# Kernel optimization log

Measured on AMD Instinct MI355X. Metric: run time of the kernel, lower is better.

## Reference

```python
import jax, jax.numpy as jnp
import numpy as np

BETA = 0.5

def setup_inputs() -> dict:
    key = jax.random.key(0)
    ks = jax.random.split(key, 10)
    B, H = 4096, 200
    ITEM, REGION = 100000, 1000
    D, HID = 128, 64  # embed_size, hidden_size
    half = D // 2
    history = jax.random.randint(ks[0], (B, H), 0, ITEM)
    target = jax.random.randint(ks[1], (B,), 0, ITEM)
    history_region = jax.random.randint(ks[2], (B, H), 0, REGION)
    target_region = jax.random.randint(ks[3], (B,), 0, REGION)
    W_hist = jax.random.normal(ks[4], (ITEM, half), jnp.float32) * 0.01
    W_tgt = jax.random.normal(ks[5], (ITEM, half), jnp.float32) * 0.01
    W_reg = jax.random.normal(ks[6], (REGION, half), jnp.float32) * 0.01
    W1 = jax.random.normal(ks[7], (D, HID), jnp.float32) * (1.0 / np.sqrt(D))
    b1 = jnp.zeros((HID,), jnp.float32)
    W2 = jax.random.normal(ks[8], (HID,), jnp.float32) * (1.0 / np.sqrt(HID))
    return {"history": history, "target": target,
            "history_region": history_region, "target_region": target_region,
            "W_hist": W_hist, "W_tgt": W_tgt, "W_reg": W_reg,
            "W1": W1, "b1": b1, "W2": W2}

def reference(history, target, history_region, target_region,
              W_hist, W_tgt, W_reg, W1, b1, W2):
    # gather + concat: [B,H,D] and [B,D]
    h = jnp.concatenate([W_hist[history], W_reg[history_region]], axis=-1)
    t = jnp.concatenate([W_tgt[target], W_reg[target_region]], axis=-1)
    inp = h * t[:, None, :]                      # [B,H,D]
    r1 = jax.nn.relu(inp @ W1 + b1)              # [B,H,HID] (dropout = identity at eval)
    logits = r1 @ W2                             # [B,H]
    mask = (history != target[:, None]).astype(logits.dtype)
    exp_A = jnp.exp(logits) * mask               # [B,H]
    exp_sum = jnp.sum(exp_A, axis=-1) ** BETA    # [B], beta-power normalization
    attn = exp_A / exp_sum[:, None]              # [B,H]
    pred = jnp.einsum('bhd,bd->b', h * attn[..., None], t)
    return jax.nn.sigmoid(pred)
```

## Files before the change

kernel.cpp:

```cpp
#include <hip/hip_runtime.h>
#include <math.h>

#define NB        4096
#define NH        200
#define HIST_ROWS 100000
#define REG_ROWS  1000
#define NTILES    13

typedef __attribute__((ext_vector_type(4))) int int4i;

#define SA 2048.0f
#define SB 16384.0f
#define ST 2048.0f
#define INV_LOGIT (1.0f / (SA * SB))
#define INV_S     (1.0f / (SA * ST))

__device__ __forceinline__ int q8(float x, float s) {
    return __float2int_rn(fminf(fmaxf(x * s, -127.f), 127.f));
}
__device__ __forceinline__ int pack4(float a, float b, float c, float d, float s) {
    const int x0 = q8(a, s), x1 = q8(b, s), x2 = q8(c, s), x3 = q8(d, s);
    return (x0 & 255) | ((x1 & 255) << 8) | ((x2 & 255) << 16) | (x3 << 24);
}

__global__ __launch_bounds__(256) void prep_all(
    const int*   __restrict__ target,
    const int*   __restrict__ target_region,
    const float* __restrict__ Wh, const float* __restrict__ Wr,
    const float* __restrict__ Wt, const float* __restrict__ W1,
    unsigned char* __restrict__ tab, signed char* __restrict__ Ball)
{
    if (blockIdx.x < NB) {
        const int b    = blockIdx.x;
        const int tgt  = target[b];
        const int treg = target_region[b];
        #pragma unroll
        for (int v = 0; v < 3; ++v) {
            const int i = threadIdx.x + v * 256;
            if (i < 640) {
                const int frag = i >> 6, nt = frag >> 1, ks = frag & 1;
                const int c = i & 63, q = c >> 4, l = c & 15;
                const float* tp = ks ? (Wr + (size_t)treg * 64) : (Wt + (size_t)tgt * 64);
                const float4 t0 = *(const float4*)(tp + q * 16);
                const float4 t1 = *(const float4*)(tp + q * 16 + 4);
                const float4 t2 = *(const float4*)(tp + q * 16 + 8);
                const float4 t3 = *(const float4*)(tp + q * 16 + 12);
                int4i ob;
                if (nt < 4) {
                    const int n = nt * 16 + l;
                    float w[16];
                    #pragma unroll
                    for (int j = 0; j < 16; ++j)
                        w[j] = W1[(ks * 64 + q * 16 + j) * 64 + n];
                    ob.x = pack4(w[0]*t0.x,  w[1]*t0.y,  w[2]*t0.z,  w[3]*t0.w,  SB);
                    ob.y = pack4(w[4]*t1.x,  w[5]*t1.y,  w[6]*t1.z,  w[7]*t1.w,  SB);
                    ob.z = pack4(w[8]*t2.x,  w[9]*t2.y,  w[10]*t2.z, w[11]*t2.w, SB);
                    ob.w = pack4(w[12]*t3.x, w[13]*t3.y, w[14]*t3.z, w[15]*t3.w, SB);
                } else {
                    if (l == 0) {
                        ob.x = pack4(t0.x, t0.y, t0.z, t0.w, ST);
                        ob.y = pack4(t1.x, t1.y, t1.z, t1.w, ST);
                        ob.z = pack4(t2.x, t2.y, t2.z, t2.w, ST);
                        ob.w = pack4(t3.x, t3.y, t3.z, t3.w, ST);
                    } else {
                        ob = (int4i){0, 0, 0, 0};
                    }
                }
                *reinterpret_cast<int4i*>(Ball + ((size_t)b * 640 + i) * 16) = ob;
            }
        }
    } else {
        const int total = (HIST_ROWS + REG_ROWS) * 16;
        const int HE    = HIST_ROWS * 16;
        unsigned* dst = (unsigned*)tab;
        for (int i = (blockIdx.x - NB) * 256 + threadIdx.x; i < total; i += 2048 * 256) {
            const float4 v = (i < HE) ? ((const float4*)Wh)[i]
                                      : ((const float4*)Wr)[i - HE];
            dst[i] = (unsigned)pack4(v.x, v.y, v.z, v.w, SA);
        }
    }
}

__device__ __forceinline__ void epi_store_i8(
    const int4i* accT, const float* w2v, const float* b1v,
    int tl, int quad, int l15, float* logit_lds, float* s_lds)
{
    float part[4] = {0.f, 0.f, 0.f, 0.f};
    #pragma unroll
    for (int nt = 0; nt < 4; ++nt)
        #pragma unroll
        for (int r = 0; r < 4; ++r)
            part[r] += fmaxf((float)accT[nt][r] * INV_LOGIT + b1v[nt], 0.f) * w2v[nt];
    #pragma unroll
    for (int r = 0; r < 4; ++r) {
        part[r] += __shfl_xor(part[r], 1);
        part[r] += __shfl_xor(part[r], 2);
        part[r] += __shfl_xor(part[r], 4);
        part[r] += __shfl_xor(part[r], 8);
    }
    if (l15 == 0) {
        const int jg = tl * 16 + quad * 4;
        #pragma unroll
        for (int r = 0; r < 4; ++r) {
            logit_lds[jg + r] = part[r];
            s_lds[jg + r]     = (float)accT[4][r] * INV_S;
        }
    }
}

__global__ __launch_bounds__(256, 3) void nais_i8s(
    const int*   __restrict__ history,
    const int*   __restrict__ target,
    const int*   __restrict__ history_region,
    const float* __restrict__ b1,
    const float* __restrict__ W2,
    const unsigned char* __restrict__ tab,
    const signed char*   __restrict__ Ball,
    float*       __restrict__ out)
{
    __shared__ float logit_lds[208];
    __shared__ float s_lds[208];
    __shared__ float red_e[4], red_p[4];

    const int b   = blockIdx.x;
    const int tid = threadIdx.x;
    const int lane = tid & 63, wv = tid >> 6;
    const int l15  = lane & 15, quad = lane >> 4;
    const int tgt  = target[b];

    const int  tls[4] = {wv, wv + 4, wv + 8, wv + 12};
    const bool has3   = (tls[3] < NTILES);

    int4i A[4][2];
    #pragma unroll
    for (int tt = 0; tt < 4; ++tt) {
        int j = ((tt == 3 && !has3) ? tls[2] : tls[tt]) * 16 + l15;
        j = j < NH ? j : NH - 1;
        const int ih = history[b * NH + j];
        const int ir = history_region[b * NH + j];
        A[tt][0] = *(const int4i*)(tab + (size_t)ih * 64 + quad * 16);
        A[tt][1] = *(const int4i*)(tab + (size_t)(HIST_ROWS + ir) * 64 + quad * 16);
    }

    int4i BF[10];
    const int4i* bp = (const int4i*)(Ball + (size_t)b * 640 * 16);
    #pragma unroll
    for (int f = 0; f < 10; ++f) BF[f] = bp[f * 64 + lane];

    float w2v[4], b1v[4];
    #pragma unroll
    for (int nt = 0; nt < 4; ++nt) {
        w2v[nt] = W2[nt * 16 + l15];
        b1v[nt] = b1[nt * 16 + l15];
    }

    #pragma unroll
    for (int pp = 0; pp < 2; ++pp) {
        const int  t0i = pp * 2, t1i = pp * 2 + 1;
        const bool hb  = (pp == 0) || has3;

        int4i acc[2][5];
        #pragma unroll
        for (int tt = 0; tt < 2; ++tt)
            #pragma unroll
            for (int nt = 0; nt < 5; ++nt) acc[tt][nt] = (int4i){0, 0, 0, 0};

        #pragma unroll
        for (int ks = 0; ks < 2; ++ks) {
            #pragma unroll
            for (int nt = 0; nt < 5; ++nt)
                acc[0][nt] = __builtin_amdgcn_mfma_i32_16x16x64_i8(
                    A[t0i][ks], BF[nt * 2 + ks], acc[0][nt], 0, 0, 0);
            if (hb) {
                #pragma unroll
                for (int nt = 0; nt < 5; ++nt)
                    acc[1][nt] = __builtin_amdgcn_mfma_i32_16x16x64_i8(
                        A[t1i][ks], BF[nt * 2 + ks], acc[1][nt], 0, 0, 0);
            }
        }

        epi_store_i8(acc[0], w2v, b1v, tls[t0i], quad, l15, logit_lds, s_lds);
        if (hb) epi_store_i8(acc[1], w2v, b1v, tls[t1i], quad, l15, logit_lds, s_lds);
    }
    __syncthreads();

    float e = 0.f, p = 0.f;
    if (tid < NH) {
        const int hj = history[b * NH + tid];
        const float ex = (hj != tgt) ? expf(logit_lds[tid]) : 0.f;
        e = ex;
        p = ex * s_lds[tid];
    }
    #pragma unroll
    for (int off = 32; off > 0; off >>= 1) {
        e += __shfl_down(e, off);
        p += __shfl_down(p, off);
    }
    if (lane == 0) { red_e[wv] = e; red_p[wv] = p; }
    __syncthreads();
    if (tid == 0) {
        const float E = red_e[0] + red_e[1] + red_e[2] + red_e[3];
        const float P = red_p[0] + red_p[1] + red_p[2] + red_p[3];
        const float pred = P / sqrtf(E);
        out[b] = 1.f / (1.f + expf(-pred));
    }
}

__device__ __forceinline__ int4i quant_row_fp32(const float* row, int quad) {
    const float4* p = (const float4*)(row + quad * 16);
    const float4 v0 = p[0], v1 = p[1], v2 = p[2], v3 = p[3];
    int4i o;
    o.x = pack4(v0.x, v0.y, v0.z, v0.w, SA);
    o.y = pack4(v1.x, v1.y, v1.z, v1.w, SA);
    o.z = pack4(v2.x, v2.y, v2.z, v2.w, SA);
    o.w = pack4(v3.x, v3.y, v3.z, v3.w, SA);
    return o;
}

__global__ __launch_bounds__(256, 3) void nais_i8_fb(
    const int*   __restrict__ history,
    const int*   __restrict__ target,
    const int*   __restrict__ history_region,
    const int*   __restrict__ target_region,
    const float* __restrict__ W_hist,
    const float* __restrict__ W_tgt,
    const float* __restrict__ W_reg,
    const float* __restrict__ W1,
    const float* __restrict__ b1,
    const float* __restrict__ W2,
    float*       __restrict__ out)
{
    __shared__ int hist_lds[224];
    __shared__ int hreg_lds[224];
    __shared__ __align__(16) float t_lds[128];
    __shared__ __align__(16) int Bf4[640 * 4];
    __shared__ float logit_lds[208];
    __shared__ float s_lds[208];
    __shared__ float red_e[4], red_p[4];

    const int b   = blockIdx.x;
    const int tid = threadIdx.x;
    const int tgt = target[b];

    if (tid < 224) {
        const int jj = tid < NH ? tid : NH - 1;
        hist_lds[tid] = history[b * NH + jj];
        hreg_lds[tid] = history_region[b * NH + jj];
    }
    if (tid < 64) {
        t_lds[tid] = W_tgt[(size_t)tgt * 64 + tid];
    } else if (tid < 128) {
        t_lds[tid] = W_reg[(size_t)target_region[b] * 64 + (tid - 64)];
    }
    __syncthreads();

    const int lane = tid & 63, wv = tid >> 6;
    const int l15  = lane & 15, quad = lane >> 4;
    const int  tls[4] = {wv, wv + 4, wv + 8, wv + 12};
    const bool has3   = (tls[3] < NTILES);

    #pragma unroll
    for (int v = 0; v < 3; ++v) {
        const int i = tid + v * 256;
        if (i < 640) {
            const int frag = i >> 6, nt = frag >> 1, ks = frag & 1;
            const int c = i & 63, q = c >> 4, l = c & 15;
            const int k0 = ks * 64 + q * 16;
            const float4 t0 = *(const float4*)(t_lds + k0);
            const float4 t1 = *(const float4*)(t_lds + k0 + 4);
            const float4 t2 = *(const float4*)(t_lds + k0 + 8);
            const float4 t3 = *(const float4*)(t_lds + k0 + 12);
            int4i ob;
            if (nt < 4) {
                const int n = nt * 16 + l;
                float w[16];
                #pragma unroll
                for (int j = 0; j < 16; ++j) w[j] = W1[(k0 + j) * 64 + n];
                ob.x = pack4(w[0]*t0.x,  w[1]*t0.y,  w[2]*t0.z,  w[3]*t0.w,  SB);
                ob.y = pack4(w[4]*t1.x,  w[5]*t1.y,  w[6]*t1.z,  w[7]*t1.w,  SB);
                ob.z = pack4(w[8]*t2.x,  w[9]*t2.y,  w[10]*t2.z, w[11]*t2.w, SB);
                ob.w = pack4(w[12]*t3.x, w[13]*t3.y, w[14]*t3.z, w[15]*t3.w, SB);
            } else {
                if (l == 0) {
                    ob.x = pack4(t0.x, t0.y, t0.z, t0.w, ST);
                    ob.y = pack4(t1.x, t1.y, t1.z, t1.w, ST);
                    ob.z = pack4(t2.x, t2.y, t2.z, t2.w, ST);
                    ob.w = pack4(t3.x, t3.y, t3.z, t3.w, ST);
                } else {
                    ob = (int4i){0, 0, 0, 0};
                }
            }
            *reinterpret_cast<int4i*>(&Bf4[i * 4]) = ob;
        }
    }
    __syncthreads();

    float w2v[4], b1v[4];
    #pragma unroll
    for (int nt = 0; nt < 4; ++nt) {
        w2v[nt] = W2[nt * 16 + l15];
        b1v[nt] = b1[nt * 16 + l15];
    }

    #pragma unroll
    for (int pp = 0; pp < 2; ++pp) {
        const int  t0i = pp * 2, t1i = pp * 2 + 1;
        const bool hb  = (pp == 0) || has3;

        int4i A[2][2];
        #pragma unroll
        for (int tt = 0; tt < 2; ++tt) {
            const int ti = t0i + tt;
            const int j  = ((ti == 3 && !has3) ? tls[2] : tls[ti]) * 16 + l15;
            A[tt][0] = quant_row_fp32(W_hist + (size_t)hist_lds[j] * 64, quad);
            A[tt][1] = quant_row_fp32(W_reg  + (size_t)hreg_lds[j] * 64, quad);
        }

        int4i acc[2][5];
        #pragma unroll
        for (int tt = 0; tt < 2; ++tt)
            #pragma unroll
            for (int nt = 0; nt < 5; ++nt) acc[tt][nt] = (int4i){0, 0, 0, 0};

        #pragma unroll
        for (int ks = 0; ks < 2; ++ks) {
            int4i bf[5];
            #pragma unroll
            for (int nt = 0; nt < 5; ++nt)
                bf[nt] = *reinterpret_cast<const int4i*>(&Bf4[((nt * 2 + ks) * 64 + lane) * 4]);
            #pragma unroll
            for (int nt = 0; nt < 5; ++nt)
                acc[0][nt] = __builtin_amdgcn_mfma_i32_16x16x64_i8(A[0][ks], bf[nt], acc[0][nt], 0, 0, 0);
            if (hb) {
                #pragma unroll
                for (int nt = 0; nt < 5; ++nt)
                    acc[1][nt] = __builtin_amdgcn_mfma_i32_16x16x64_i8(A[1][ks], bf[nt], acc[1][nt], 0, 0, 0);
            }
        }

        epi_store_i8(acc[0], w2v, b1v, tls[t0i], quad, l15, logit_lds, s_lds);
        if (hb) epi_store_i8(acc[1], w2v, b1v, tls[t1i], quad, l15, logit_lds, s_lds);
    }
    __syncthreads();

    float e = 0.f, p = 0.f;
    if (tid < NH) {
        const float ex = (hist_lds[tid] != tgt) ? expf(logit_lds[tid]) : 0.f;
        e = ex;
        p = ex * s_lds[tid];
    }
    #pragma unroll
    for (int off = 32; off > 0; off >>= 1) {
        e += __shfl_down(e, off);
        p += __shfl_down(p, off);
    }
    if (lane == 0) { red_e[wv] = e; red_p[wv] = p; }
    __syncthreads();
    if (tid == 0) {
        const float E = red_e[0] + red_e[1] + red_e[2] + red_e[3];
        const float P = red_p[0] + red_p[1] + red_p[2] + red_p[3];
        const float pred = P / sqrtf(E);
        out[b] = 1.f / (1.f + expf(-pred));
    }
}

extern "C" void kernel_launch(void* const* d_in, const int* in_sizes, int n_in,
                              void* d_out, int out_size, void* d_ws, size_t ws_size,
                              hipStream_t stream) {
    const int*   history        = (const int*)  d_in[0];
    const int*   target         = (const int*)  d_in[1];
    const int*   history_region = (const int*)  d_in[2];
    const int*   target_region  = (const int*)  d_in[3];
    const float* W_hist         = (const float*)d_in[4];
    const float* W_tgt          = (const float*)d_in[5];
    const float* W_reg          = (const float*)d_in[6];
    const float* W1             = (const float*)d_in[7];
    const float* b1             = (const float*)d_in[8];
    const float* W2             = (const float*)d_in[9];
    float* out = (float*)d_out;

    const size_t tab_bytes  = (size_t)(HIST_ROWS + REG_ROWS) * 64;
    const size_t ball_bytes = (size_t)NB * 640 * 16;
    if (ws_size >= tab_bytes + ball_bytes) {
        unsigned char* tab  = (unsigned char*)d_ws;
        signed char*   Ball = (signed char*)d_ws + tab_bytes;
        prep_all<<<NB + 2048, 256, 0, stream>>>(target, target_region,
                                                W_hist, W_reg, W_tgt, W1, tab, Ball);
        nais_i8s<<<NB, 256, 0, stream>>>(history, target, history_region,
                                         b1, W2, tab, Ball, out);
    } else {
        nais_i8_fb<<<NB, 256, 0, stream>>>(history, target, history_region, target_region,
                                           W_hist, W_tgt, W_reg, W1, b1, W2, out);
    }
}
```

Measured before the change: 148.1 us.

## Use one wavefront per batch row with prefetched tiles; stage W1 in LDS

The main kernel now runs one 64-lane wavefront per batch row instead of four. It loops over the 13 history tiles two at a time and prefetches the next pair of gathered rows while the current MFMAs run, which removes the block-level __syncthreads and the cross-wave reduction. The prep kernel also copies W1 into shared memory before building the per-target B fragments, so the strided global reads of W1 become LDS reads. In exchange each block does serial work across seven iterations, so there is less parallelism per row, and prep blocks now use 32KB of LDS, which may reduce their occupancy.

```diff
diff --git a/kernel.cpp b/kernel.cpp
--- a/kernel.cpp
+++ b/kernel.cpp
@@ -31,9 +31,16 @@
     unsigned char* __restrict__ tab, signed char* __restrict__ Ball)
 {
     if (blockIdx.x < NB) {
+        __shared__ __align__(16) float W1s[128 * 64];
         const int b    = blockIdx.x;
         const int tgt  = target[b];
         const int treg = target_region[b];
+        #pragma unroll
+        for (int v = 0; v < 8; ++v) {
+            const int i4 = threadIdx.x + v * 256;
+            ((float4*)W1s)[i4] = ((const float4*)W1)[i4];
+        }
+        __syncthreads();
         #pragma unroll
         for (int v = 0; v < 3; ++v) {
             const int i = threadIdx.x + v * 256;
@@ -51,7 +58,7 @@
                     float w[16];
                     #pragma unroll
                     for (int j = 0; j < 16; ++j)
-                        w[j] = W1[(ks * 64 + q * 16 + j) * 64 + n];
+                        w[j] = W1s[(ks * 64 + q * 16 + j) * 64 + n];
                     ob.x = pack4(w[0]*t0.x,  w[1]*t0.y,  w[2]*t0.z,  w[3]*t0.w,  SB);
                     ob.y = pack4(w[4]*t1.x,  w[5]*t1.y,  w[6]*t1.z,  w[7]*t1.w,  SB);
                     ob.z = pack4(w[8]*t2.x,  w[9]*t2.y,  w[10]*t2.z, w[11]*t2.w, SB);
@@ -108,7 +115,7 @@
     }
 }
 
-__global__ __launch_bounds__(256, 3) void nais_i8s(
+__global__ __launch_bounds__(64, 3) void nais_i8w(
     const int*   __restrict__ history,
     const int*   __restrict__ target,
     const int*   __restrict__ history_region,
@@ -120,30 +127,14 @@
 {
     __shared__ float logit_lds[208];
     __shared__ float s_lds[208];
-    __shared__ float red_e[4], red_p[4];
-
-    const int b   = blockIdx.x;
-    const int tid = threadIdx.x;
-    const int lane = tid & 63, wv = tid >> 6;
+
+    const int b    = blockIdx.x;
+    const int lane = threadIdx.x;
     const int l15  = lane & 15, quad = lane >> 4;
     const int tgt  = target[b];
 
-    const int  tls[4] = {wv, wv + 4, wv + 8, wv + 12};
-    const bool has3   = (tls[3] < NTILES);
-
-    int4i A[4][2];
-    #pragma unroll
-    for (int tt = 0; tt < 4; ++tt) {
-        int j = ((tt == 3 && !has3) ? tls[2] : tls[tt]) * 16 + l15;
-        j = j < NH ? j : NH - 1;
-        const int ih = history[b * NH + j];
-        const int ir = history_region[b * NH + j];
-        A[tt][0] = *(const int4i*)(tab + (size_t)ih * 64 + quad * 16);
-        A[tt][1] = *(const int4i*)(tab + (size_t)(HIST_ROWS + ir) * 64 + quad * 16);
-    }
-
     int4i BF[10];
-    const int4i* bp = (const int4i*)(Ball + (size_t)b * 640 * 16);
+    const int4i* bp = (const int4i*)(Ball + (size_t)b * 10240);
     #pragma unroll
     for (int f = 0; f < 10; ++f) BF[f] = bp[f * 64 + lane];
 
@@ -154,10 +145,35 @@
         b1v[nt] = b1[nt * 16 + l15];
     }
 
-    #pragma unroll
-    for (int pp = 0; pp < 2; ++pp) {
-        const int  t0i = pp * 2, t1i = pp * 2 + 1;
-        const bool hb  = (pp == 0) || has3;
+    int4i Ac[2][2], An[2][2];
+    {
+        #pragma unroll
+        for (int tt = 0; tt < 2; ++tt) {
+            const int j  = tt * 16 + l15;
+            const int ih = history[b * NH + j];
+            const int ir = history_region[b * NH + j];
+            Ac[tt][0] = *(const int4i*)(tab + (size_t)ih * 64 + quad * 16);
+            Ac[tt][1] = *(const int4i*)(tab + (size_t)(HIST_ROWS + ir) * 64 + quad * 16);
+        }
+    }
+
+    #pragma unroll 1
+    for (int p = 0; p < 7; ++p) {
+        const int  tl0 = p * 2, tl1 = tl0 + 1;
+        const bool h1  = (tl1 < NTILES);
+
+        if (p < 6) {
+            #pragma unroll
+            for (int tt = 0; tt < 2; ++tt) {
+                const int ntl = tl0 + 2 + tt;
+                int j = (ntl < NTILES ? ntl : NTILES - 1) * 16 + l15;
+                j = j < NH ? j : NH - 1;
+                const int ih = history[b * NH + j];
+                const int ir = history_region[b * NH + j];
+                An[tt][0] = *(const int4i*)(tab + (size_t)ih * 64 + quad * 16);
+                An[tt][1] = *(const int4i*)(tab + (size_t)(HIST_ROWS + ir) * 64 + quad * 16);
+            }
+        }
 
         int4i acc[2][5];
         #pragma unroll
@@ -170,38 +186,42 @@
             #pragma unroll
             for (int nt = 0; nt < 5; ++nt)
                 acc[0][nt] = __builtin_amdgcn_mfma_i32_16x16x64_i8(
-                    A[t0i][ks], BF[nt * 2 + ks], acc[0][nt], 0, 0, 0);
-            if (hb) {
+                    Ac[0][ks], BF[nt * 2 + ks], acc[0][nt], 0, 0, 0);
+            if (h1) {
                 #pragma unroll
                 for (int nt = 0; nt < 5; ++nt)
                     acc[1][nt] = __builtin_amdgcn_mfma_i32_16x16x64_i8(
-                        A[t1i][ks], BF[nt * 2 + ks], acc[1][nt], 0, 0, 0);
+                        Ac[1][ks], BF[nt * 2 + ks], acc[1][nt], 0, 0, 0);
             }
         }
 
-        epi_store_i8(acc[0], w2v, b1v, tls[t0i], quad, l15, logit_lds, s_lds);
-        if (hb) epi_store_i8(acc[1], w2v, b1v, tls[t1i], quad, l15, logit_lds, s_lds);
-    }
-    __syncthreads();
-
-    float e = 0.f, p = 0.f;
-    if (tid < NH) {
-        const int hj = history[b * NH + tid];
-        const float ex = (hj != tgt) ? expf(logit_lds[tid]) : 0.f;
-        e = ex;
-        p = ex * s_lds[tid];
+        epi_store_i8(acc[0], w2v, b1v, tl0, quad, l15, logit_lds, s_lds);
+        if (h1) epi_store_i8(acc[1], w2v, b1v, tl1, quad, l15, logit_lds, s_lds);
+
+        #pragma unroll
+        for (int tt = 0; tt < 2; ++tt)
+            #pragma unroll
+            for (int ks = 0; ks < 2; ++ks) Ac[tt][ks] = An[tt][ks];
+    }
+
+    float e = 0.f, pr = 0.f;
+    #pragma unroll
+    for (int v = 0; v < 4; ++v) {
+        const int idx = lane + v * 64;
+        if (idx < NH) {
+            const int hj = history[b * NH + idx];
+            const float ex = (hj != tgt) ? expf(logit_lds[idx]) : 0.f;
+            e  += ex;
+            pr += ex * s_lds[idx];
+        }
     }
     #pragma unroll
     for (int off = 32; off > 0; off >>= 1) {
-        e += __shfl_down(e, off);
-        p += __shfl_down(p, off);
-    }
-    if (lane == 0) { red_e[wv] = e; red_p[wv] = p; }
-    __syncthreads();
-    if (tid == 0) {
-        const float E = red_e[0] + red_e[1] + red_e[2] + red_e[3];
-        const float P = red_p[0] + red_p[1] + red_p[2] + red_p[3];
-        const float pred = P / sqrtf(E);
+        e  += __shfl_down(e, off);
+        pr += __shfl_down(pr, off);
+    }
+    if (lane == 0) {
+        const float pred = pr / sqrtf(e);
         out[b] = 1.f / (1.f + expf(-pred));
     }
 }
@@ -386,8 +406,8 @@
         signed char*   Ball = (signed char*)d_ws + tab_bytes;
         prep_all<<<NB + 2048, 256, 0, stream>>>(target, target_region,
                                                 W_hist, W_reg, W_tgt, W1, tab, Ball);
-        nais_i8s<<<NB, 256, 0, stream>>>(history, target, history_region,
-                                         b1, W2, tab, Ball, out);
+        nais_i8w<<<NB, 64, 0, stream>>>(history, target, history_region,
+                                        b1, W2, tab, Ball, out);
     } else {
         nais_i8_fb<<<NB, 256, 0, stream>>>(history, target, history_region, target_region,
                                            W_hist, W_tgt, W_reg, W1, b1, W2, out);
```

Result: slower. 155.9 us (+5.2%).
